# Performance work log

Hardware: AMD Instinct MI355X
Metric: run time of the kernel (lower is better)

## Reference

```python
import jax, jax.numpy as jnp
import numpy as np

NUM_HEADS = 16
NUM_KV_HEADS = 4
HEAD_DIM = 128
HALF_DIM = HEAD_DIM // 2
LAMBDA_INIT = 0.8
LAMBDA_MIN = 0.0
LAMBDA_MAX = 1.0
CAUSAL = True
NORMALIZE_DIFF = True
NEG = -1.0e9


def setup_inputs() -> dict:
    key = jax.random.key(0)
    k1, k2, k3 = jax.random.split(key, 3)
    B, Sq, Sk = 1, 2048, 2048
    query = jax.random.normal(k1, (B, NUM_HEADS, Sq, HEAD_DIM), dtype=jnp.float32)
    key_t = jax.random.normal(k2, (B, NUM_KV_HEADS, Sk, HEAD_DIM), dtype=jnp.float32)
    value = jax.random.normal(k3, (B, NUM_KV_HEADS, Sk, HEAD_DIM), dtype=jnp.float32)
    return {"query": query, "key": key_t, "value": value}


def reference(query, key, value):
    scale = 1.0 / (HALF_DIM ** 0.5)
    lam = jnp.clip(jnp.float32(LAMBDA_INIT), LAMBDA_MIN, LAMBDA_MAX)
    # GQA: repeat KV heads to match query heads
    rep = NUM_HEADS // NUM_KV_HEADS
    k = jnp.repeat(key, rep, axis=1)    # [b,h,k,d]
    v = jnp.repeat(value, rep, axis=1)  # [b,h,k,d]
    q1, q2 = query[..., :HALF_DIM], query[..., HALF_DIM:]
    k1, k2 = k[..., :HALF_DIM], k[..., HALF_DIM:]
    scores1 = jnp.einsum('bhqd,bhkd->bhqk', q1, k1) * scale
    scores2 = jnp.einsum('bhqd,bhkd->bhqk', q2, k2) * scale
    if CAUSAL:
        Sq, Sk = query.shape[2], k.shape[2]
        mask = jnp.tril(jnp.ones((Sq, Sk), dtype=jnp.float32))  # lower-triangular causal
        scores1 = scores1 * mask + (1.0 - mask) * NEG
        scores2 = scores2 * mask + (1.0 - mask) * NEG
    attn1 = jax.nn.softmax(scores1, axis=-1)
    attn2 = jax.nn.softmax(scores2, axis=-1)
    diff_attn = attn1 - lam * attn2
    out = jnp.einsum('bhqk,bhkd->bhqd', diff_attn, v)
    if NORMALIZE_DIFF:
        out = out * (1.0 - LAMBDA_INIT)
    return out
```

## Files before the change

kernel.cpp:

```cpp
#include <hip/hip_runtime.h>

#define NUM_HEADS 16
#define HEAD_DIM  128
#define SEQ       2048
#define KT_STRIDE 8192

typedef __attribute__((ext_vector_type(8))) unsigned short us8;
typedef __attribute__((ext_vector_type(8))) __bf16 bf16x8;
typedef __attribute__((ext_vector_type(4))) float f32x4;
typedef __attribute__((ext_vector_type(16))) float f32x16;
typedef __attribute__((ext_vector_type(4))) unsigned u32x4;
typedef __attribute__((ext_vector_type(2))) unsigned u32x2;

static __device__ inline unsigned short f2bf(float x) {
    union { float f; unsigned u; } v; v.f = x;
    unsigned r = v.u + 0x7FFFu + ((v.u >> 16) & 1u);
    return (unsigned short)(r >> 16);
}
static __device__ inline unsigned pk2bf(float a, float b) {
    return (unsigned)f2bf(a) | ((unsigned)f2bf(b) << 16);
}
static __device__ inline float fast_exp2(float x) {
#if __has_builtin(__builtin_amdgcn_exp2f)
    return __builtin_amdgcn_exp2f(x);
#else
    return exp2f(x);
#endif
}
static __device__ inline unsigned pack_hi(unsigned clo, unsigned chi) {
#if __has_builtin(__builtin_amdgcn_perm)
    return __builtin_amdgcn_perm(chi, clo, 0x07060302u);
#else
    return (clo >> 16) | (chi & 0xffff0000u);
#endif
}
static __device__ inline f32x16 mfma32(us8 a, us8 b, f32x16 c) {
    return __builtin_amdgcn_mfma_f32_32x32x16_bf16(
        __builtin_bit_cast(bf16x8, a), __builtin_bit_cast(bf16x8, b), c, 0, 0, 0);
}

__global__ __launch_bounds__(256)
void prep_frag(const float* __restrict__ K, const float* __restrict__ V,
               unsigned short* __restrict__ KF, unsigned short* __restrict__ VF)
{
    const int bx  = (int)blockIdx.x, t = (int)threadIdx.x;
    const int which = bx & 1, khb = (bx >> 1) & 1, kt = (bx >> 2) & 31, kvh = bx >> 7;
    __shared__ __align__(16) float Ls[32][132];

    const float* src = (which ? V : K) + ((size_t)kvh * SEQ + kt * 64 + khb * 32) * HEAD_DIM;
    #pragma unroll
    for (int i = 0; i < 4; ++i) {
        const int idx = t + i * 256;
        const int r = idx >> 5, c4 = idx & 31;
        *(float4*)&Ls[r][c4 * 4] = *(const float4*)(src + (size_t)r * HEAD_DIM + c4 * 4);
    }
    __syncthreads();

    if (!which) {
        #pragma unroll
        for (int i = 0; i < 2; ++i) {
            const int c = t + i * 256;
            const int lane = c & 63, ds = (c >> 6) & 3, mat = (c >> 8) & 1;
            const int H = lane >> 5;
            const int row = lane & 31;
            const int dim = mat * 64 + ds * 16 + H * 8;
            u32x4 pk;
            #pragma unroll
            for (int jj = 0; jj < 4; ++jj)
                pk[jj] = pk2bf(Ls[row][dim + 2*jj], Ls[row][dim + 2*jj + 1]);
            *(us8*)(KF + ((size_t)(kvh * 32 + kt) * 16 + khb * 8 + mat * 4 + ds) * 512 + lane * 8)
                = __builtin_bit_cast(us8, pk);
        }
    } else {
        #pragma unroll
        for (int i = 0; i < 2; ++i) {
            const int c = t + i * 256;
            const int lane = c & 63, db = (c >> 6) & 3, ks = (c >> 8) & 1;
            const int H = lane >> 5;
            const int s0 = ks * 16 + H * 8;
            const int d  = db * 32 + (lane & 31);
            u32x4 pk;
            #pragma unroll
            for (int jj = 0; jj < 4; ++jj)
                pk[jj] = pk2bf(Ls[s0 + 2*jj][d], Ls[s0 + 2*jj + 1][d]);
            *(us8*)(VF + ((size_t)(kvh * 32 + kt) * 16 + khb * 8 + ks * 4 + db) * 512 + lane * 8)
                = __builtin_bit_cast(us8, pk);
        }
    }
}

__global__ __launch_bounds__(512, 2)
void diff_attn_mfma15(const float* __restrict__ Q,
                      const unsigned short* __restrict__ KF,
                      const unsigned short* __restrict__ VF,
                      float* __restrict__ Out)
{
    __shared__ __align__(16) unsigned short KV[2][16384];
    __shared__ float cb[2][2][32][136];
    __shared__ float rsb[2][2][2][32];

    const int t    = (int)threadIdx.x;
    const int wv   = t >> 6;
    const int ln   = t & 63;
    const int qsel = wv >> 2;
    const int mat  = (wv >> 1) & 1;
    const int kh   = wv & 1;
    const int q    = ln & 31;
    const int H    = ln >> 5;

    const int bx  = (int)blockIdx.x;
    const int xcd = bx & 7;
    const int u   = bx >> 3;
    const int kvh = xcd >> 1;
    const int h   = kvh * 4 + (u & 3);
    const int ss  = (u >> 2) | ((xcd & 1) << 3);

    const unsigned short* sgb = (wv < 4 ? KF : VF)
        + ((size_t)kvh * 32 * 16 + (wv & 3) * 4) * 512 + ln * 8;
    auto stage = [&](int jt, int b) {
        const unsigned short* tb = sgb + (size_t)jt * KT_STRIDE;
        #pragma unroll
        for (int i = 0; i < 4; ++i) {
            __builtin_amdgcn_global_load_lds(
                (const __attribute__((address_space(1))) unsigned int*)(tb + i * 512),
                (__attribute__((address_space(3))) unsigned int*)&KV[b][(wv * 4 + i) * 512],
                16, 0, 0);
        }
    };

    const int kbase = (kh * 8 + mat * 4) * 512;
    const int vbase = (16 + kh * 8) * 512;

    const float qscale = 0.125f * 1.44269504088896340736f;

    us8 qhi[4];
    auto loadQ = [&](int q0c) {
        const float* qr = Q + ((size_t)h * SEQ + q0c + q) * HEAD_DIM + mat * 64;
        #pragma unroll
        for (int ds = 0; ds < 4; ++ds) {
            const int d0 = ds * 16 + H * 8;
            float x[8];
            *(float4*)&x[0] = *(const float4*)(qr + d0);
            *(float4*)&x[4] = *(const float4*)(qr + d0 + 4);
            us8 hi8;
            #pragma unroll
            for (int j = 0; j < 8; ++j) hi8[j] = f2bf(x[j] * qscale);
            qhi[ds] = hi8;
        }
    };

    f32x16 o[4];
    f32x4  rsv;

    auto make_bp = [&](const f32x16& sv, int rbase, int kg0, int qg, bool dmask) -> us8 {
        unsigned c0[8];
        if (dmask) {
            #pragma unroll
            for (int r = 0; r < 8; ++r) {
                const int ri = rbase + r;
                const int kg = kg0 + (ri & 3) + ((ri >> 2) << 3);
                float e = (kg <= qg) ? fast_exp2(sv[ri]) : 0.f;
                c0[r] = __builtin_bit_cast(unsigned, e);
            }
        } else {
            #pragma unroll
            for (int r = 0; r < 8; ++r)
                c0[r] = __builtin_bit_cast(unsigned, fast_exp2(sv[rbase + r]));
        }
        const unsigned pA = pack_hi(c0[0], c0[1]);
        const unsigned pB = pack_hi(c0[2], c0[3]);
        const unsigned pC = pack_hi(c0[4], c0[5]);
        const unsigned pD = pack_hi(c0[6], c0[7]);
        rsv[0] += __builtin_bit_cast(float, pA << 16);
        rsv[1] += __builtin_bit_cast(float, pA & 0xffff0000u);
        rsv[2] += __builtin_bit_cast(float, pB << 16);
        rsv[3] += __builtin_bit_cast(float, pB & 0xffff0000u);
        rsv[0] += __builtin_bit_cast(float, pC << 16);
        rsv[1] += __builtin_bit_cast(float, pC & 0xffff0000u);
        rsv[2] += __builtin_bit_cast(float, pD << 16);
        rsv[3] += __builtin_bit_cast(float, pD & 0xffff0000u);
        u32x4 bw;
#if __has_builtin(__builtin_amdgcn_permlane32_swap)
        {
            u32x2 r02 = __builtin_amdgcn_permlane32_swap(pA, pC, false, false);
            u32x2 r13 = __builtin_amdgcn_permlane32_swap(pB, pD, false, false);
            bw[0] = r02[0]; bw[1] = r13[0]; bw[2] = r02[1]; bw[3] = r13[1];
        }
#else
        {
            const unsigned x1 = H ? pA : pC;
            const unsigned x2 = H ? pB : pD;
            const unsigned t1 = (unsigned)__shfl_xor((int)x1, 32, 64);
            const unsigned t2 = (unsigned)__shfl_xor((int)x2, 32, 64);
            bw[0] = H ? t1 : pA;
            bw[1] = H ? t2 : pB;
            bw[2] = H ? pC : t1;
            bw[3] = H ? pD : t2;
        }
#endif
        return __builtin_bit_cast(us8, bw);
    };

    auto epilogue = [&](int q0c) {
        __syncthreads();
        {
            float rsc = (rsv[0] + rsv[1]) + (rsv[2] + rsv[3]);
            rsc += __shfl_xor(rsc, 32, 64);
            if (ln < 32) rsb[qsel][mat][kh][ln] = rsc;
        }
        if (kh == 1) {
            #pragma unroll
            for (int db = 0; db < 4; ++db)
                #pragma unroll
                for (int i = 0; i < 4; ++i) {
                    float4 v = { o[db][i*4+0], o[db][i*4+1], o[db][i*4+2], o[db][i*4+3] };
                    *(float4*)&cb[qsel][mat][q][db * 32 + 8 * i + 4 * H] = v;
                }
        }
        __syncthreads();
        if (kh == 0) {
            const float l = rsb[qsel][mat][0][q] + rsb[qsel][mat][1][q];
            const float a = mat ? (0.16f / l) : (0.2f / l);
            #pragma unroll
            for (int db = 0; db < 4; ++db)
                #pragma unroll
                for (int i = 0; i < 4; ++i) {
                    float4 v = *(float4*)&cb[qsel][mat][q][db * 32 + 8 * i + 4 * H];
                    o[db][i*4+0] = (o[db][i*4+0] + v.x) * a;
                    o[db][i*4+1] = (o[db][i*4+1] + v.y) * a;
                    o[db][i*4+2] = (o[db][i*4+2] + v.z) * a;
                    o[db][i*4+3] = (o[db][i*4+3] + v.w) * a;
                }
            if (mat == 1) {
                #pragma unroll
                for (int db = 0; db < 4; ++db)
                    #pragma unroll
                    for (int i = 0; i < 4; ++i) {
                        float4 v = { o[db][i*4+0], o[db][i*4+1], o[db][i*4+2], o[db][i*4+3] };
                        *(float4*)&cb[qsel][1][q][db * 32 + 8 * i + 4 * H] = v;
                    }
            }
        }
        __syncthreads();
        if (mat == 0 && kh == 0) {
            float* ob = Out + ((size_t)h * SEQ + q0c + q) * HEAD_DIM;
            #pragma unroll
            for (int db = 0; db < 4; ++db)
                #pragma unroll
                for (int i = 0; i < 4; ++i) {
                    float4 v = *(float4*)&cb[qsel][1][q][db * 32 + 8 * i + 4 * H];
                    float4 r;
                    r.x = o[db][i*4+0] - v.x;
                    r.y = o[db][i*4+1] - v.y;
                    r.z = o[db][i*4+2] - v.z;
                    r.w = o[db][i*4+3] - v.w;
                    *(float4*)(ob + db * 32 + 8 * i + 4 * H) = r;
                }
        }
    };

    int bufc = 0;

    auto run_pair = [&](int p, int nextp) {
        const int nseg = p + 1;
        const int q0   = p * 64 + qsel * 32;
        loadQ(q0);
        #pragma unroll
        for (int i = 0; i < 4; ++i) o[i] = (f32x16)0.f;
        rsv = (f32x4)0.f;

        for (int j = 0; j < nseg; ++j) {
            if (j + 1 < nseg)      stage(j + 1, bufc ^ 1);
            else if (nextp >= 0)   stage(0,     bufc ^ 1);

            const unsigned short* bufp = KV[bufc];
            us8 kaf[4];
            #pragma unroll
            for (int ds = 0; ds < 4; ++ds)
                kaf[ds] = *(const us8*)&bufp[kbase + ds * 512 + ln * 8];
            us8 va[8];
            #pragma unroll
            for (int c = 0; c < 8; ++c)
                va[c] = *(const us8*)&bufp[vbase + c * 512 + ln * 8];

            f32x16 s = (f32x16)0.f;
            #pragma unroll
            for (int ds = 0; ds < 4; ++ds) s = mfma32(kaf[ds], qhi[ds], s);

            const bool last = (j == nseg - 1);
            const int  kg0  = j * 64 + kh * 32 + 4 * H;
            const int  qg   = q0 + q;

            us8 bp = make_bp(s, 0, kg0, qg, last);
            #pragma unroll
            for (int db = 0; db < 4; ++db) o[db] = mfma32(va[db], bp, o[db]);
            bp = make_bp(s, 8, kg0, qg, last);
            #pragma unroll
            for (int db = 0; db < 4; ++db) o[db] = mfma32(va[4 + db], bp, o[db]);

            __syncthreads();
            bufc ^= 1;
        }
        epilogue(p * 64 + qsel * 32);
    };

    stage(0, bufc);
    __syncthreads();

    run_pair(31 - ss, ss);
    run_pair(ss, -1);
}

extern "C" void kernel_launch(void* const* d_in, const int* in_sizes, int n_in,
                              void* d_out, int out_size, void* d_ws, size_t ws_size,
                              hipStream_t stream) {
    const float* Q = (const float*)d_in[0];
    const float* K = (const float*)d_in[1];
    const float* V = (const float*)d_in[2];
    float* Out = (float*)d_out;

    unsigned short* KF = (unsigned short*)d_ws;
    unsigned short* VF = KF + (size_t)4 * SEQ * HEAD_DIM;

    prep_frag<<<512, 256, 0, stream>>>(K, V, KF, VF);
    diff_attn_mfma15<<<256, 512, 0, stream>>>(Q, KF, VF, Out);
}
```

Baseline: 117.8 us.

## Triple-buffer KV staging with single barrier per step and alias epilogue buffer

Replaces the double-buffered KV staging, which had a trailing __syncthreads per iteration, with a three-slot ring. Each iteration waits only on the current slot using vmcnt and takes one s_barrier, so the next tile's loads overlap compute with one fewer barrier. The epilogue scratch buffer now aliases the KV shared memory, keeping LDS use near its old size despite the third buffer. The QK score MFMA chain is split into two independent accumulators to shorten the dependency chain. In exchange, the first tile of each query pair is no longer prefetched across pairs, and correctness depends on the hand-placed vmcnt(4) matching the number of loads issued by stage.

```diff
diff --git a/kernel.cpp b/kernel.cpp
--- a/kernel.cpp
+++ b/kernel.cpp
@@ -90,14 +90,15 @@
 }
 
 __global__ __launch_bounds__(512, 2)
-void diff_attn_mfma15(const float* __restrict__ Q,
+void diff_attn_mfma16(const float* __restrict__ Q,
                       const unsigned short* __restrict__ KF,
                       const unsigned short* __restrict__ VF,
                       float* __restrict__ Out)
 {
-    __shared__ __align__(16) unsigned short KV[2][16384];
-    __shared__ float cb[2][2][32][136];
+    __shared__ __align__(16) unsigned short KV[3][16384];
     __shared__ float rsb[2][2][2][32];
+    float* cbf = (float*)&KV[0][0];
+#define CB(qs, m, qq, ii) cbf[((((qs) * 2 + (m)) * 32 + (qq)) * 136) + (ii)]
 
     const int t    = (int)threadIdx.x;
     const int wv   = t >> 6;
@@ -152,20 +153,23 @@
     f32x16 o[4];
     f32x4  rsv;
 
-    auto make_bp = [&](const f32x16& sv, int rbase, int kg0, int qg, bool dmask) -> us8 {
+    auto make_bp = [&](const f32x16& sv, const f32x16& sw, int rbase, int kg0, int qg,
+                       bool dmask) -> us8 {
         unsigned c0[8];
         if (dmask) {
             #pragma unroll
             for (int r = 0; r < 8; ++r) {
                 const int ri = rbase + r;
                 const int kg = kg0 + (ri & 3) + ((ri >> 2) << 3);
-                float e = (kg <= qg) ? fast_exp2(sv[ri]) : 0.f;
+                float e = (kg <= qg) ? fast_exp2(sv[ri] + sw[ri]) : 0.f;
                 c0[r] = __builtin_bit_cast(unsigned, e);
             }
         } else {
             #pragma unroll
-            for (int r = 0; r < 8; ++r)
-                c0[r] = __builtin_bit_cast(unsigned, fast_exp2(sv[rbase + r]));
+            for (int r = 0; r < 8; ++r) {
+                const int ri = rbase + r;
+                c0[r] = __builtin_bit_cast(unsigned, fast_exp2(sv[ri] + sw[ri]));
+            }
         }
         const unsigned pA = pack_hi(c0[0], c0[1]);
         const unsigned pB = pack_hi(c0[2], c0[3]);
@@ -214,7 +218,7 @@
                 #pragma unroll
                 for (int i = 0; i < 4; ++i) {
                     float4 v = { o[db][i*4+0], o[db][i*4+1], o[db][i*4+2], o[db][i*4+3] };
-                    *(float4*)&cb[qsel][mat][q][db * 32 + 8 * i + 4 * H] = v;
+                    *(float4*)&CB(qsel, mat, q, db * 32 + 8 * i + 4 * H) = v;
                 }
         }
         __syncthreads();
@@ -225,7 +229,7 @@
             for (int db = 0; db < 4; ++db)
                 #pragma unroll
                 for (int i = 0; i < 4; ++i) {
-                    float4 v = *(float4*)&cb[qsel][mat][q][db * 32 + 8 * i + 4 * H];
+                    float4 v = *(float4*)&CB(qsel, mat, q, db * 32 + 8 * i + 4 * H);
                     o[db][i*4+0] = (o[db][i*4+0] + v.x) * a;
                     o[db][i*4+1] = (o[db][i*4+1] + v.y) * a;
                     o[db][i*4+2] = (o[db][i*4+2] + v.z) * a;
@@ -237,7 +241,7 @@
                     #pragma unroll
                     for (int i = 0; i < 4; ++i) {
                         float4 v = { o[db][i*4+0], o[db][i*4+1], o[db][i*4+2], o[db][i*4+3] };
-                        *(float4*)&cb[qsel][1][q][db * 32 + 8 * i + 4 * H] = v;
+                        *(float4*)&CB(qsel, 1, q, db * 32 + 8 * i + 4 * H) = v;
                     }
             }
         }
@@ -248,7 +252,7 @@
             for (int db = 0; db < 4; ++db)
                 #pragma unroll
                 for (int i = 0; i < 4; ++i) {
-                    float4 v = *(float4*)&cb[qsel][1][q][db * 32 + 8 * i + 4 * H];
+                    float4 v = *(float4*)&CB(qsel, 1, q, db * 32 + 8 * i + 4 * H);
                     float4 r;
                     r.x = o[db][i*4+0] - v.x;
                     r.y = o[db][i*4+1] - v.y;
@@ -259,9 +263,7 @@
         }
     };
 
-    int bufc = 0;
-
-    auto run_pair = [&](int p, int nextp) {
+    auto run_pair = [&](int p) {
         const int nseg = p + 1;
         const int q0   = p * 64 + qsel * 32;
         loadQ(q0);
@@ -269,11 +271,26 @@
         for (int i = 0; i < 4; ++i) o[i] = (f32x16)0.f;
         rsv = (f32x4)0.f;
 
+        __syncthreads();
+        stage(0, 0);
+        asm volatile("s_waitcnt vmcnt(0)" ::: "memory");
+        __builtin_amdgcn_sched_barrier(0);
+        __builtin_amdgcn_s_barrier();
+        __builtin_amdgcn_sched_barrier(0);
+
+        int cur = 0;
         for (int j = 0; j < nseg; ++j) {
-            if (j + 1 < nseg)      stage(j + 1, bufc ^ 1);
-            else if (nextp >= 0)   stage(0,     bufc ^ 1);
-
-            const unsigned short* bufp = KV[bufc];
+            if (j + 1 < nseg) {
+                stage(j + 1, (cur + 1) % 3);
+                asm volatile("s_waitcnt vmcnt(4)" ::: "memory");
+            } else {
+                asm volatile("s_waitcnt vmcnt(0)" ::: "memory");
+            }
+            __builtin_amdgcn_sched_barrier(0);
+            __builtin_amdgcn_s_barrier();
+            __builtin_amdgcn_sched_barrier(0);
+
+            const unsigned short* bufp = &KV[cur][0];
             us8 kaf[4];
             #pragma unroll
             for (int ds = 0; ds < 4; ++ds)
@@ -283,32 +300,32 @@
             for (int c = 0; c < 8; ++c)
                 va[c] = *(const us8*)&bufp[vbase + c * 512 + ln * 8];
 
-            f32x16 s = (f32x16)0.f;
-            #pragma unroll
-            for (int ds = 0; ds < 4; ++ds) s = mfma32(kaf[ds], qhi[ds], s);
+            f32x16 s  = (f32x16)0.f;
+            f32x16 s2 = (f32x16)0.f;
+            s  = mfma32(kaf[0], qhi[0], s);
+            s2 = mfma32(kaf[2], qhi[2], s2);
+            s  = mfma32(kaf[1], qhi[1], s);
+            s2 = mfma32(kaf[3], qhi[3], s2);
 
             const bool last = (j == nseg - 1);
             const int  kg0  = j * 64 + kh * 32 + 4 * H;
             const int  qg   = q0 + q;
 
-            us8 bp = make_bp(s, 0, kg0, qg, last);
+            us8 bp = make_bp(s, s2, 0, kg0, qg, last);
             #pragma unroll
             for (int db = 0; db < 4; ++db) o[db] = mfma32(va[db], bp, o[db]);
-            bp = make_bp(s, 8, kg0, qg, last);
+            bp = make_bp(s, s2, 8, kg0, qg, last);
             #pragma unroll
             for (int db = 0; db < 4; ++db) o[db] = mfma32(va[4 + db], bp, o[db]);
 
-            __syncthreads();
-            bufc ^= 1;
-        }
-        epilogue(p * 64 + qsel * 32);
-    };
-
-    stage(0, bufc);
-    __syncthreads();
-
-    run_pair(31 - ss, ss);
-    run_pair(ss, -1);
+            cur = (cur + 1) % 3;
+        }
+        epilogue(q0);
+    };
+
+    run_pair(31 - ss);
+    run_pair(ss);
+#undef CB
 }
 
 extern "C" void kernel_launch(void* const* d_in, const int* in_sizes, int n_in,
@@ -323,5 +340,5 @@
     unsigned short* VF = KF + (size_t)4 * SEQ * HEAD_DIM;
 
     prep_frag<<<512, 256, 0, stream>>>(K, V, KF, VF);
-    diff_attn_mfma15<<<256, 512, 0, stream>>>(Q, KF, VF, Out);
-}
+    diff_attn_mfma16<<<256, 512, 0, stream>>>(Q, KF, VF, Out);
+}
```

Result: faster. 113.8 us (-3.4%).
